# Performance work log

Measured on AMD Instinct MI355X. Metric: run time of the kernel, lower is better.

The kernel has to match this reference:

```python
import jax, jax.numpy as jnp
import numpy as np

THRESHOLD = 0.5
NEG_POS_RATIO = 3
ALPHA = 1.0
B, A, C, M = 128, 8732, 21, 8


def cxcy_to_xy(c):
    return jnp.concatenate([c[:, :2] - c[:, 2:] / 2.0, c[:, :2] + c[:, 2:] / 2.0], axis=1)


def cxcy_to_gcxgcy(cxcy, priors):
    g_cxcy = (cxcy[:, :2] - priors[:, :2]) / (priors[:, 2:] / 10.0)
    g_wh = jnp.log(cxcy[:, 2:] / priors[:, 2:]) * 5.0
    return jnp.concatenate([g_cxcy, g_wh], axis=1)


def find_jaccard_overlap(a, b):
    # a: [M,4] xy, b: [A,4] xy -> IoU [M,A]
    lt = jnp.maximum(a[:, None, :2], b[None, :, :2])
    rb = jnp.minimum(a[:, None, 2:], b[None, :, 2:])
    wh = jnp.clip(rb - lt, 0.0)
    inter = wh[..., 0] * wh[..., 1]
    area_a = (a[:, 2] - a[:, 0]) * (a[:, 3] - a[:, 1])
    area_b = (b[:, 2] - b[:, 0]) * (b[:, 3] - b[:, 1])
    return inter / (area_a[:, None] + area_b[None, :] - inter)


def setup_inputs() -> dict:
    key = jax.random.key(0)
    k1, k2, k3, k4, k5, k6 = jax.random.split(key, 6)
    predicted_locs = jax.random.normal(k1, (B, A, 4), dtype=jnp.float32)
    predicted_scores = jax.random.normal(k2, (B, A, C), dtype=jnp.float32)
    # ground-truth boxes in xy pixel coords within [0, 300], guaranteed x2>x1, y2>y1
    u = jax.random.uniform(k3, (B, M, 4), dtype=jnp.float32)
    x1y1 = u[..., :2] * 150.0
    x2y2 = x1y1 + u[..., 2:] * 140.0 + 10.0
    boxes = jnp.concatenate([x1y1, x2y2], axis=-1)
    labels = jax.random.randint(k4, (B, M), 1, C)  # 1..20, never background
    # anchor boxes in cxcy, w/h strictly positive
    cxcy = jax.random.uniform(k5, (A, 2), dtype=jnp.float32)
    wh = 0.05 + 0.95 * jax.random.uniform(k6, (A, 2), dtype=jnp.float32)
    anchor_boxes = jnp.concatenate([cxcy, wh], axis=1)
    return {"predicted_locs": predicted_locs, "predicted_scores": predicted_scores,
            "boxes": boxes, "labels": labels, "anchor_boxes": anchor_boxes}


def _match(boxes_i, labels_i, anchors_cxcy, anchors_xy):
    # boxes_i: [M,4] xy pixels, labels_i: [M]
    scaled = boxes_i / 300.0
    iou = find_jaccard_overlap(scaled, anchors_xy)            # [M, A]
    obj_for_anchor = jnp.argmax(iou, axis=0)                  # [A]
    iou_for_anchor = jnp.max(iou, axis=0)                     # [A]
    anchor_for_obj = jnp.argmax(iou, axis=1)                  # [M]
    obj_for_anchor = obj_for_anchor.at[anchor_for_obj].set(jnp.arange(M))
    iou_for_anchor = iou_for_anchor.at[anchor_for_obj].set(1.0)
    label_for_anchor = labels_i[obj_for_anchor]               # [A]
    label_for_anchor = jnp.where(iou_for_anchor < THRESHOLD, 0, label_for_anchor)
    true_locs = cxcy_to_gcxgcy(boxes_i[obj_for_anchor], anchors_cxcy)  # [A,4]
    return label_for_anchor, true_locs


def reference(predicted_locs, predicted_scores, boxes, labels, anchor_boxes):
    anchors_xy = cxcy_to_xy(anchor_boxes)
    true_classes, true_locs = jax.vmap(_match, in_axes=(0, 0, None, None))(
        boxes, labels, anchor_boxes, anchors_xy)              # [B,A], [B,A,4]

    pos = true_classes != 0                                   # [B,A]
    n_pos = pos.sum(axis=1)                                   # [B]
    n_pos_total = n_pos.sum()

    # L1Loss(mean) over positive anchors' 4 coords
    l1 = jnp.abs(predicted_locs - true_locs)                  # [B,A,4]
    loc_loss = (l1 * pos[..., None]).sum() / (n_pos_total.astype(jnp.float32) * 4.0)

    # per-anchor cross entropy
    logp = jax.nn.log_softmax(predicted_scores, axis=-1)      # [B,A,C]
    ce = -jnp.take_along_axis(logp, true_classes[..., None], axis=-1)[..., 0]  # [B,A]

    conf_pos = (ce * pos).sum()
    ce_neg = jnp.where(pos, 0.0, ce)
    ce_neg_sorted = -jnp.sort(-ce_neg, axis=1)                # descending per row
    ranks = jnp.arange(A)[None, :]
    hard = ranks < (NEG_POS_RATIO * n_pos)[:, None]
    conf_hard_neg = (ce_neg_sorted * hard).sum()

    conf_loss = (conf_hard_neg + conf_pos) / n_pos_total.astype(jnp.float32)
    return conf_loss + ALPHA * loc_loss
```

## Files before the change

### kernel.cpp

```cpp
#include <hip/hip_runtime.h>
#include <hip/hip_bf16.h>

constexpr int B = 128;
constexpr int A = 8732;
constexpr int C = 21;
constexpr int M = 8;

__global__ void k_init(float* accf, int* npt) {
    int t = threadIdx.x;
    if (t < 3) accf[t] = 0.f;
    if (t == 3) *npt = 0;
}

__global__ __launch_bounds__(1024) void k_match(
    const float* __restrict__ boxes,
    const int*   __restrict__ labels,
    const float* __restrict__ anchors,
    int*         __restrict__ packed,
    int*         __restrict__ n_pos,
    int*         __restrict__ npt)
{
    __shared__ float         s_iou[A];
    __shared__ unsigned char s_obj[A];
    __shared__ float s_pv[M][16];
    __shared__ int   s_pi[M][16];
    __shared__ int   s_force[M];
    __shared__ int   s_c[16];
    __shared__ float s_box[M][4];
    __shared__ int   s_lab[M];

    const int b = blockIdx.x;
    const int t = threadIdx.x;
    const int lane = t & 63;
    const int wv   = t >> 6;

    if (t < M * 4) ((float*)s_box)[t] = boxes[b * M * 4 + t];
    if (t < M)     s_lab[t] = labels[b * M + t];
    __syncthreads();

    float bb[M][4], barea[M];
#pragma unroll
    for (int m = 0; m < M; m++) {
        bb[m][0] = s_box[m][0] / 300.f;
        bb[m][1] = s_box[m][1] / 300.f;
        bb[m][2] = s_box[m][2] / 300.f;
        bb[m][3] = s_box[m][3] / 300.f;
        barea[m] = (bb[m][2] - bb[m][0]) * (bb[m][3] - bb[m][1]);
    }

    float bestv[M];
    int   besti[M];
#pragma unroll
    for (int m = 0; m < M; m++) { bestv[m] = -1.f; besti[m] = 0; }

    const float4* anch4 = (const float4*)anchors;
    for (int a = t; a < A; a += 1024) {
        float4 an = anch4[a];
        float ax1 = an.x - an.z / 2.0f, ay1 = an.y - an.w / 2.0f;
        float ax2 = an.x + an.z / 2.0f, ay2 = an.y + an.w / 2.0f;
        float aarea = (ax2 - ax1) * (ay2 - ay1);

        float bmax = -1.f; int bm = 0;
#pragma unroll
        for (int m = 0; m < M; m++) {
            float lx = fmaxf(bb[m][0], ax1), ly = fmaxf(bb[m][1], ay1);
            float rx = fminf(bb[m][2], ax2), ry = fminf(bb[m][3], ay2);
            float iw = fmaxf(rx - lx, 0.f), ih = fmaxf(ry - ly, 0.f);
            float inter = iw * ih;
            float iou = inter / (barea[m] + aarea - inter);
            if (iou > bmax) { bmax = iou; bm = m; }
            if (iou > bestv[m]) { bestv[m] = iou; besti[m] = a; }
        }
        s_iou[a] = bmax;
        s_obj[a] = (unsigned char)bm;
    }

#pragma unroll
    for (int m = 0; m < M; m++) {
        float v = bestv[m]; int i = besti[m];
        for (int off = 32; off > 0; off >>= 1) {
            float ov = __shfl_down(v, off);
            int   oi = __shfl_down(i, off);
            if (ov > v || (ov == v && oi < i)) { v = ov; i = oi; }
        }
        if (lane == 0) { s_pv[m][wv] = v; s_pi[m][wv] = i; }
    }
    __syncthreads();

    if (t < M) {
        float bv = -1.f; int bi = 0x7fffffff;
#pragma unroll
        for (int w = 0; w < 16; w++) {
            float v = s_pv[t][w]; int i = s_pi[t][w];
            if (v > bv || (v == bv && i < bi)) { bv = v; bi = i; }
        }
        s_force[t] = bi;
    }
    __syncthreads();

    if (t == 0) {
        for (int m = 0; m < M; m++) {
            int a = s_force[m];
            s_obj[a] = (unsigned char)m;
            s_iou[a] = 1.0f;
        }
    }
    __syncthreads();

    int cnt = 0;
    for (int a = t; a < A; a += 1024) {
        int obj = s_obj[a];
        int lab = s_lab[obj];
        if (s_iou[a] < 0.5f) lab = 0;
        packed[(size_t)b * A + a] = lab | (obj << 8);
        if (lab != 0) cnt++;
    }
    for (int off = 32; off > 0; off >>= 1) cnt += __shfl_down(cnt, off);
    if (lane == 0) s_c[wv] = cnt;
    __syncthreads();
    if (t == 0) {
        int c0 = 0;
#pragma unroll
        for (int w = 0; w < 16; w++) c0 += s_c[w];
        n_pos[b] = c0;
        atomicAdd(npt, c0);
    }
}

__global__ __launch_bounds__(256) void k_ce(
    const float* __restrict__ plocs,
    const float* __restrict__ pscores,
    const float* __restrict__ boxes,
    const float* __restrict__ anchors,
    int*         __restrict__ buf,
    float*       __restrict__ accf)
{
    constexpr int NQ = B * A / 4;
    const int i4 = blockIdx.x * 256 + threadIdx.x;
    float l_pos = 0.f, l_loc = 0.f;

    if (i4 < NQ) {
        const int base = i4 * 4;
        const float4* s4 = (const float4*)(pscores + (size_t)base * C);
        float4 v[21];
#pragma unroll
        for (int i = 0; i < 21; i++) v[i] = s4[i];
        const float* f = (const float*)v;

        int4 pk4 = ((const int4*)buf)[i4];
        const int pks[4] = {pk4.x, pk4.y, pk4.z, pk4.w};

        const int b = base / A;
        const int a0 = base - b * A;

        float4 cn4;
        float* cn = (float*)&cn4;
#pragma unroll
        for (int j = 0; j < 4; j++) {
            const float* row = f + j * C;
            const int lab = pks[j] & 255;
            const int obj = pks[j] >> 8;

            float mx = row[0];
#pragma unroll
            for (int c = 1; c < C; c++) mx = fmaxf(mx, row[c]);
            float sum = 0.f, slab = 0.f;
#pragma unroll
            for (int c = 0; c < C; c++) {
                sum += __expf(row[c] - mx);
                if (c == lab) slab = row[c];
            }
            float ce = mx + __logf(sum) - slab;

            cn[j] = ce;
            if (lab != 0) {
                cn[j] = 0.f;
                l_pos += ce;
                const float* bx = boxes + ((size_t)b * M + obj) * 4;
                const float* an = anchors + (size_t)(a0 + j) * 4;
                float dx = (bx[0] - an[0]) / (an[2] / 10.f);
                float dy = (bx[1] - an[1]) / (an[3] / 10.f);
                float dw = logf(bx[2] / an[2]) * 5.f;
                float dh = logf(bx[3] / an[3]) * 5.f;
                float4 p = ((const float4*)plocs)[base + j];
                l_loc += fabsf(p.x - dx) + fabsf(p.y - dy) +
                         fabsf(p.z - dw) + fabsf(p.w - dh);
            }
        }
        ((float4*)buf)[i4] = cn4;
    }

    for (int off = 32; off > 0; off >>= 1) {
        l_pos += __shfl_down(l_pos, off);
        l_loc += __shfl_down(l_loc, off);
    }
    if ((threadIdx.x & 63) == 0 && (l_pos != 0.f || l_loc != 0.f)) {
        atomicAdd(&accf[0], l_pos);
        atomicAdd(&accf[1], l_loc);
    }
}

__global__ __launch_bounds__(1024) void k_topk(
    const float* __restrict__ ce_neg,
    const int*   __restrict__ n_pos,
    float*       __restrict__ accf)
{
    __shared__ unsigned int vals[A];
    __shared__ unsigned int hist[256];
    __shared__ unsigned int s_prefix, s_krem;
    __shared__ float        rs[16];
    __shared__ unsigned int rc[16];

    const int b = blockIdx.x;
    const int t = threadIdx.x;
    const int lane = t & 63;
    const int wv   = t >> 6;
    const int K = 3 * n_pos[b];
    const float* row = ce_neg + (size_t)b * A;

    {
        const uint4* r4 = (const uint4*)row;
        uint4* v4 = (uint4*)vals;
        for (int i = t; i < A / 4; i += 1024) v4[i] = r4[i];
    }
    if (t == 0) { s_prefix = 0u; s_krem = (unsigned)K; }
    __syncthreads();

    if (K <= 0) return;

    if (K >= A) {
        float s = 0.f;
        for (int i = t; i < A; i += 1024) s += __uint_as_float(vals[i]);
        for (int off = 32; off > 0; off >>= 1) s += __shfl_down(s, off);
        if (lane == 0) rs[wv] = s;
        __syncthreads();
        if (t == 0) {
            float tot = 0.f;
#pragma unroll
            for (int w = 0; w < 16; w++) tot += rs[w];
            atomicAdd(&accf[2], tot);
        }
        return;
    }

    for (int pass = 0; pass < 4; pass++) {
        const int shift = 24 - 8 * pass;
        const unsigned pref = s_prefix;
        const unsigned krem = s_krem;
        if (t < 256) hist[t] = 0u;
        __syncthreads();
        for (int i = t; i < A; i += 1024) {
            unsigned int v = vals[i];
            if (pass == 0 || (v >> (shift + 8)) == pref)
                atomicAdd(&hist[(v >> shift) & 255u], 1u);
        }
        __syncthreads();
        if (t < 64) {
            unsigned h0 = hist[4 * t + 0], h1 = hist[4 * t + 1];
            unsigned h2 = hist[4 * t + 2], h3 = hist[4 * t + 3];
            unsigned s3 = h3, s2 = h2 + s3, s1 = h1 + s2, s0 = h0 + s1;
            unsigned suf = s0;
            for (int off = 1; off < 64; off <<= 1) {
                unsigned o = __shfl_down(suf, off);
                if (t + off < 64) suf += o;
            }
            unsigned above = suf - s0;
            hist[4 * t + 0] = above + s0;
            hist[4 * t + 1] = above + s1;
            hist[4 * t + 2] = above + s2;
            hist[4 * t + 3] = above + s3;
        }
        __syncthreads();
        if (t < 256) {
            unsigned ssT = hist[t];
            unsigned ssN = (t < 255) ? hist[t + 1] : 0u;
            if (ssT >= krem && ssN < krem) {
                s_prefix = (pref << 8) | (unsigned)t;
                s_krem   = krem - ssN;
            }
        }
        __syncthreads();
    }

    const unsigned int tb = s_prefix;
    float sg = 0.f; unsigned int cg = 0;
    for (int i = t; i < A; i += 1024) {
        unsigned int v = vals[i];
        if (v > tb) { sg += __uint_as_float(v); cg++; }
    }
    for (int off = 32; off > 0; off >>= 1) {
        sg += __shfl_down(sg, off);
        cg += __shfl_down(cg, off);
    }
    if (lane == 0) { rs[wv] = sg; rc[wv] = cg; }
    __syncthreads();
    if (t == 0) {
        float tv = __uint_as_float(tb);
        float tot = 0.f; unsigned cnt = 0;
#pragma unroll
        for (int w = 0; w < 16; w++) { tot += rs[w]; cnt += rc[w]; }
        atomicAdd(&accf[2], tot + (float)(K - (int)cnt) * tv);
    }
}

__global__ void k_final(const float* __restrict__ accf,
                        const int* __restrict__ npt,
                        float* __restrict__ out)
{
    float n = (float)(*npt);
    float conf_loss = (accf[2] + accf[0]) / n;
    float loc_loss  = accf[1] / (n * 4.f);
    out[0] = conf_loss + loc_loss;
}

extern "C" void kernel_launch(void* const* d_in, const int* in_sizes, int n_in,
                              void* d_out, int out_size, void* d_ws, size_t ws_size,
                              hipStream_t stream)
{
    const float* plocs   = (const float*)d_in[0];
    const float* pscores = (const float*)d_in[1];
    const float* boxes   = (const float*)d_in[2];
    const int*   labels  = (const int*)d_in[3];
    const float* anchors = (const float*)d_in[4];
    float*       out     = (float*)d_out;

    float* accf  = (float*)d_ws;
    int*   npt   = (int*)d_ws + 3;
    int*   n_pos = (int*)d_ws + 8;
    int*   buf   = (int*)d_ws + 8 + B;

    k_init<<<1, 64, 0, stream>>>(accf, npt);
    k_match<<<B, 1024, 0, stream>>>(boxes, labels, anchors, buf, n_pos, npt);
    constexpr int NQ = B * A / 4;
    k_ce<<<(NQ + 255) / 256, 256, 0, stream>>>(plocs, pscores, boxes, anchors, buf, accf);
    k_topk<<<B, 1024, 0, stream>>>((const float*)buf, n_pos, accf);
    k_final<<<1, 1, 0, stream>>>(accf, npt, out);
}
```

Before: 290.7 us.

## Stage score rows through shared memory with coalesced loads, one anchor per thread

The CE kernel now cooperatively copies each block's contiguous 256-anchor slab of class scores into LDS using coalesced float4 loads, then each thread computes log-softmax CE for a single anchor from shared memory. This replaces per-thread strided 84-float register loads that coalesced poorly. It adds a block barrier and about 21KB of LDS per block, which may limit occupancy, and quadruples the thread count.

```diff
diff --git a/kernel.cpp b/kernel.cpp
--- a/kernel.cpp
+++ b/kernel.cpp
@@ -135,66 +135,60 @@
     int*         __restrict__ buf,
     float*       __restrict__ accf)
 {
-    constexpr int NQ = B * A / 4;
-    const int i4 = blockIdx.x * 256 + threadIdx.x;
+    __shared__ float s[256 * C];
+
+    const int t    = threadIdx.x;
+    const int flat = blockIdx.x * 256 + t;
+
+    {
+        const float4* g4 = (const float4*)(pscores + (size_t)blockIdx.x * (256 * C));
+        float4* s4 = (float4*)s;
+#pragma unroll
+        for (int i = 0; i < 6; i++) {
+            const int idx = t + i * 256;
+            if (idx < (256 * C) / 4) s4[idx] = g4[idx];
+        }
+    }
+    __syncthreads();
+
     float l_pos = 0.f, l_loc = 0.f;
 
-    if (i4 < NQ) {
-        const int base = i4 * 4;
-        const float4* s4 = (const float4*)(pscores + (size_t)base * C);
-        float4 v[21];
-#pragma unroll
-        for (int i = 0; i < 21; i++) v[i] = s4[i];
-        const float* f = (const float*)v;
-
-        int4 pk4 = ((const int4*)buf)[i4];
-        const int pks[4] = {pk4.x, pk4.y, pk4.z, pk4.w};
-
-        const int b = base / A;
-        const int a0 = base - b * A;
-
-        float4 cn4;
-        float* cn = (float*)&cn4;
-#pragma unroll
-        for (int j = 0; j < 4; j++) {
-            const float* row = f + j * C;
-            const int lab = pks[j] & 255;
-            const int obj = pks[j] >> 8;
-
-            float mx = row[0];
-#pragma unroll
-            for (int c = 1; c < C; c++) mx = fmaxf(mx, row[c]);
-            float sum = 0.f, slab = 0.f;
-#pragma unroll
-            for (int c = 0; c < C; c++) {
-                sum += __expf(row[c] - mx);
-                if (c == lab) slab = row[c];
-            }
-            float ce = mx + __logf(sum) - slab;
-
-            cn[j] = ce;
-            if (lab != 0) {
-                cn[j] = 0.f;
-                l_pos += ce;
-                const float* bx = boxes + ((size_t)b * M + obj) * 4;
-                const float* an = anchors + (size_t)(a0 + j) * 4;
-                float dx = (bx[0] - an[0]) / (an[2] / 10.f);
-                float dy = (bx[1] - an[1]) / (an[3] / 10.f);
-                float dw = logf(bx[2] / an[2]) * 5.f;
-                float dh = logf(bx[3] / an[3]) * 5.f;
-                float4 p = ((const float4*)plocs)[base + j];
-                l_loc += fabsf(p.x - dx) + fabsf(p.y - dy) +
-                         fabsf(p.z - dw) + fabsf(p.w - dh);
-            }
-        }
-        ((float4*)buf)[i4] = cn4;
-    }
+    const float* row = s + t * C;
+    const int pk  = buf[flat];
+    const int lab = pk & 255;
+    const int obj = pk >> 8;
+
+    float mx = row[0];
+#pragma unroll
+    for (int c = 1; c < C; c++) mx = fmaxf(mx, row[c]);
+    float sum = 0.f;
+#pragma unroll
+    for (int c = 0; c < C; c++) sum += __expf(row[c] - mx);
+    const float ce = mx + __logf(sum) - row[lab];
+
+    float cn = ce;
+    if (lab != 0) {
+        cn = 0.f;
+        l_pos = ce;
+        const int b = flat / A;
+        const int a = flat - b * A;
+        const float* bx = boxes + ((size_t)b * M + obj) * 4;
+        const float* an = anchors + (size_t)a * 4;
+        float dx = (bx[0] - an[0]) / (an[2] / 10.f);
+        float dy = (bx[1] - an[1]) / (an[3] / 10.f);
+        float dw = logf(bx[2] / an[2]) * 5.f;
+        float dh = logf(bx[3] / an[3]) * 5.f;
+        float4 p = ((const float4*)plocs)[flat];
+        l_loc = fabsf(p.x - dx) + fabsf(p.y - dy) +
+                fabsf(p.z - dw) + fabsf(p.w - dh);
+    }
+    ((float*)buf)[flat] = cn;
 
     for (int off = 32; off > 0; off >>= 1) {
         l_pos += __shfl_down(l_pos, off);
         l_loc += __shfl_down(l_loc, off);
     }
-    if ((threadIdx.x & 63) == 0 && (l_pos != 0.f || l_loc != 0.f)) {
+    if ((t & 63) == 0 && (l_pos != 0.f || l_loc != 0.f)) {
         atomicAdd(&accf[0], l_pos);
         atomicAdd(&accf[1], l_loc);
     }
@@ -331,8 +325,8 @@
 
     k_init<<<1, 64, 0, stream>>>(accf, npt);
     k_match<<<B, 1024, 0, stream>>>(boxes, labels, anchors, buf, n_pos, npt);
-    constexpr int NQ = B * A / 4;
-    k_ce<<<(NQ + 255) / 256, 256, 0, stream>>>(plocs, pscores, boxes, anchors, buf, accf);
+    constexpr int NB = (B * A) / 256;
+    k_ce<<<NB, 256, 0, stream>>>(plocs, pscores, boxes, anchors, buf, accf);
     k_topk<<<B, 1024, 0, stream>>>((const float*)buf, n_pos, accf);
     k_final<<<1, 1, 0, stream>>>(accf, npt, out);
 }
```

Result: slower. 440.6 us (+51.6%).

## Fold init and final kernels into neighbours; use per-wave histograms in top-k

Applied to the files above, without the earlier changes.

Removes the separate init and final kernel launches. Accumulator zeroing moves into k_match block 0, the n_pos total is computed in k_ce block 0, and the last k_topk block (found with a done counter) computes the output. The radix-select histogram in k_topk now uses per-wave shared histograms that are summed afterwards, to reduce LDS atomic contention. This costs extra shared memory and one more reduction step per pass. Zeroing inside k_match is safe only because the accumulators are not used until later kernels in the stream.

```diff
diff --git a/kernel.cpp b/kernel.cpp
--- a/kernel.cpp
+++ b/kernel.cpp
@@ -6,11 +6,6 @@
 constexpr int C = 21;
 constexpr int M = 8;
 
-__global__ void k_init(float* accf, int* npt) {
-    int t = threadIdx.x;
-    if (t < 3) accf[t] = 0.f;
-    if (t == 3) *npt = 0;
-}
 
 __global__ __launch_bounds__(1024) void k_match(
     const float* __restrict__ boxes,
@@ -18,7 +13,8 @@
     const float* __restrict__ anchors,
     int*         __restrict__ packed,
     int*         __restrict__ n_pos,
-    int*         __restrict__ npt)
+    float*       __restrict__ accf,
+    int*         __restrict__ done)
 {
     __shared__ float         s_iou[A];
     __shared__ unsigned char s_obj[A];
@@ -34,6 +30,10 @@
     const int lane = t & 63;
     const int wv   = t >> 6;
 
+    if (b == 0 && t == 0) {
+        accf[0] = 0.f; accf[1] = 0.f; accf[2] = 0.f; *done = 0;
+    }
+
     if (t < M * 4) ((float*)s_box)[t] = boxes[b * M * 4 + t];
     if (t < M)     s_lab[t] = labels[b * M + t];
     __syncthreads();
@@ -123,7 +123,6 @@
 #pragma unroll
         for (int w = 0; w < 16; w++) c0 += s_c[w];
         n_pos[b] = c0;
-        atomicAdd(npt, c0);
     }
 }
 
@@ -133,8 +132,16 @@
     const float* __restrict__ boxes,
     const float* __restrict__ anchors,
     int*         __restrict__ buf,
-    float*       __restrict__ accf)
+    float*       __restrict__ accf,
+    const int*   __restrict__ n_pos,
+    int*         __restrict__ npt)
 {
+    if (blockIdx.x == 0 && threadIdx.x < 64) {
+        int v = n_pos[threadIdx.x] + n_pos[threadIdx.x + 64];
+        for (int off = 32; off > 0; off >>= 1) v += __shfl_down(v, off);
+        if (threadIdx.x == 0) *npt = v;
+    }
+
     constexpr int NQ = B * A / 4;
     const int i4 = blockIdx.x * 256 + threadIdx.x;
     float l_pos = 0.f, l_loc = 0.f;
@@ -203,10 +210,14 @@
 __global__ __launch_bounds__(1024) void k_topk(
     const float* __restrict__ ce_neg,
     const int*   __restrict__ n_pos,
-    float*       __restrict__ accf)
+    const int*   __restrict__ npt,
+    float*       __restrict__ accf,
+    int*         __restrict__ done,
+    float*       __restrict__ out)
 {
     __shared__ unsigned int vals[A];
     __shared__ unsigned int hist[256];
+    __shared__ unsigned int whist[16][257];
     __shared__ unsigned int s_prefix, s_krem;
     __shared__ float        rs[16];
     __shared__ unsigned int rc[16];
@@ -226,7 +237,7 @@
     if (t == 0) { s_prefix = 0u; s_krem = (unsigned)K; }
     __syncthreads();
 
-    if (K <= 0) return;
+    float blockSum = 0.f;
 
     if (K >= A) {
         float s = 0.f;
@@ -238,79 +249,89 @@
             float tot = 0.f;
 #pragma unroll
             for (int w = 0; w < 16; w++) tot += rs[w];
-            atomicAdd(&accf[2], tot);
-        }
-        return;
-    }
-
-    for (int pass = 0; pass < 4; pass++) {
-        const int shift = 24 - 8 * pass;
-        const unsigned pref = s_prefix;
-        const unsigned krem = s_krem;
-        if (t < 256) hist[t] = 0u;
-        __syncthreads();
+            blockSum = tot;
+        }
+    } else if (K > 0) {
+        for (int pass = 0; pass < 4; pass++) {
+            const int shift = 24 - 8 * pass;
+            const unsigned pref = s_prefix;
+            const unsigned krem = s_krem;
+            unsigned* wf = &whist[0][0];
+            for (int i = t; i < 16 * 257; i += 1024) wf[i] = 0u;
+            __syncthreads();
+            for (int i = t; i < A; i += 1024) {
+                unsigned int v = vals[i];
+                if (pass == 0 || (v >> (shift + 8)) == pref)
+                    atomicAdd(&whist[wv][(v >> shift) & 255u], 1u);
+            }
+            __syncthreads();
+            if (t < 256) {
+                unsigned s = 0;
+#pragma unroll
+                for (int w = 0; w < 16; w++) s += whist[w][t];
+                hist[t] = s;
+            }
+            __syncthreads();
+            if (t < 64) {
+                unsigned h0 = hist[4 * t + 0], h1 = hist[4 * t + 1];
+                unsigned h2 = hist[4 * t + 2], h3 = hist[4 * t + 3];
+                unsigned s3 = h3, s2 = h2 + s3, s1 = h1 + s2, s0 = h0 + s1;
+                unsigned suf = s0;
+                for (int off = 1; off < 64; off <<= 1) {
+                    unsigned o = __shfl_down(suf, off);
+                    if (t + off < 64) suf += o;
+                }
+                unsigned above = suf - s0;
+                hist[4 * t + 0] = above + s0;
+                hist[4 * t + 1] = above + s1;
+                hist[4 * t + 2] = above + s2;
+                hist[4 * t + 3] = above + s3;
+            }
+            __syncthreads();
+            if (t < 256) {
+                unsigned ssT = hist[t];
+                unsigned ssN = (t < 255) ? hist[t + 1] : 0u;
+                if (ssT >= krem && ssN < krem) {
+                    s_prefix = (pref << 8) | (unsigned)t;
+                    s_krem   = krem - ssN;
+                }
+            }
+            __syncthreads();
+        }
+
+        const unsigned int tb = s_prefix;
+        float sg = 0.f; unsigned int cg = 0;
         for (int i = t; i < A; i += 1024) {
             unsigned int v = vals[i];
-            if (pass == 0 || (v >> (shift + 8)) == pref)
-                atomicAdd(&hist[(v >> shift) & 255u], 1u);
-        }
+            if (v > tb) { sg += __uint_as_float(v); cg++; }
+        }
+        for (int off = 32; off > 0; off >>= 1) {
+            sg += __shfl_down(sg, off);
+            cg += __shfl_down(cg, off);
+        }
+        if (lane == 0) { rs[wv] = sg; rc[wv] = cg; }
         __syncthreads();
-        if (t < 64) {
-            unsigned h0 = hist[4 * t + 0], h1 = hist[4 * t + 1];
-            unsigned h2 = hist[4 * t + 2], h3 = hist[4 * t + 3];
-            unsigned s3 = h3, s2 = h2 + s3, s1 = h1 + s2, s0 = h0 + s1;
-            unsigned suf = s0;
-            for (int off = 1; off < 64; off <<= 1) {
-                unsigned o = __shfl_down(suf, off);
-                if (t + off < 64) suf += o;
-            }
-            unsigned above = suf - s0;
-            hist[4 * t + 0] = above + s0;
-            hist[4 * t + 1] = above + s1;
-            hist[4 * t + 2] = above + s2;
-            hist[4 * t + 3] = above + s3;
-        }
-        __syncthreads();
-        if (t < 256) {
-            unsigned ssT = hist[t];
-            unsigned ssN = (t < 255) ? hist[t + 1] : 0u;
-            if (ssT >= krem && ssN < krem) {
-                s_prefix = (pref << 8) | (unsigned)t;
-                s_krem   = krem - ssN;
-            }
-        }
-        __syncthreads();
-    }
-
-    const unsigned int tb = s_prefix;
-    float sg = 0.f; unsigned int cg = 0;
-    for (int i = t; i < A; i += 1024) {
-        unsigned int v = vals[i];
-        if (v > tb) { sg += __uint_as_float(v); cg++; }
-    }
-    for (int off = 32; off > 0; off >>= 1) {
-        sg += __shfl_down(sg, off);
-        cg += __shfl_down(cg, off);
-    }
-    if (lane == 0) { rs[wv] = sg; rc[wv] = cg; }
-    __syncthreads();
+        if (t == 0) {
+            float tv = __uint_as_float(tb);
+            float tot = 0.f; unsigned cnt = 0;
+#pragma unroll
+            for (int w = 0; w < 16; w++) { tot += rs[w]; cnt += rc[w]; }
+            blockSum = tot + (float)(K - (int)cnt) * tv;
+        }
+    }
+
     if (t == 0) {
-        float tv = __uint_as_float(tb);
-        float tot = 0.f; unsigned cnt = 0;
-#pragma unroll
-        for (int w = 0; w < 16; w++) { tot += rs[w]; cnt += rc[w]; }
-        atomicAdd(&accf[2], tot + (float)(K - (int)cnt) * tv);
-    }
-}
-
-__global__ void k_final(const float* __restrict__ accf,
-                        const int* __restrict__ npt,
-                        float* __restrict__ out)
-{
-    float n = (float)(*npt);
-    float conf_loss = (accf[2] + accf[0]) / n;
-    float loc_loss  = accf[1] / (n * 4.f);
-    out[0] = conf_loss + loc_loss;
+        if (blockSum != 0.f) atomicAdd(&accf[2], blockSum);
+        __threadfence();
+        unsigned old = atomicAdd((unsigned*)done, 1u);
+        if (old == (unsigned)(B - 1)) {
+            float cpos = atomicAdd(&accf[0], 0.f);
+            float lsum = atomicAdd(&accf[1], 0.f);
+            float chn  = atomicAdd(&accf[2], 0.f);
+            float n = (float)(*npt);
+            out[0] = (chn + cpos) / n + lsum / (n * 4.f);
+        }
+    }
 }
 
 extern "C" void kernel_launch(void* const* d_in, const int* in_sizes, int n_in,
@@ -325,14 +346,14 @@
     float*       out     = (float*)d_out;
 
     float* accf  = (float*)d_ws;
-    int*   npt   = (int*)d_ws + 3;
+    int*   done  = (int*)d_ws + 3;
+    int*   npt   = (int*)d_ws + 4;
     int*   n_pos = (int*)d_ws + 8;
     int*   buf   = (int*)d_ws + 8 + B;
 
-    k_init<<<1, 64, 0, stream>>>(accf, npt);
-    k_match<<<B, 1024, 0, stream>>>(boxes, labels, anchors, buf, n_pos, npt);
+    k_match<<<B, 1024, 0, stream>>>(boxes, labels, anchors, buf, n_pos, accf, done);
     constexpr int NQ = B * A / 4;
-    k_ce<<<(NQ + 255) / 256, 256, 0, stream>>>(plocs, pscores, boxes, anchors, buf, accf);
-    k_topk<<<B, 1024, 0, stream>>>((const float*)buf, n_pos, accf);
-    k_final<<<1, 1, 0, stream>>>(accf, npt, out);
+    k_ce<<<(NQ + 255) / 256, 256, 0, stream>>>(plocs, pscores, boxes, anchors,
+                                               buf, accf, n_pos, npt);
+    k_topk<<<B, 1024, 0, stream>>>((const float*)buf, n_pos, npt, accf, done, out);
 }
```

Result: no change. 289.5 us (-0.4%).
